# Optimization experiments

Measured on AMD Instinct MI355X. Metric: run time of the kernel, lower is better.

## Reference

```python
import jax, jax.numpy as jnp
import numpy as np

T, D, H, E, TOP_K = 4096, 512, 2048, 16, 2


def setup_inputs() -> dict:
    key = jax.random.key(0)
    ks = jax.random.split(key, 4)
    x = jax.random.normal(ks[0], (T, D), dtype=jnp.float32)
    Wg = jax.random.normal(ks[1], (D, E), dtype=jnp.float32) * 0.02
    bg = jnp.zeros((E,), dtype=jnp.float32)
    W1 = jax.random.normal(ks[2], (E, D, H), dtype=jnp.float32) * 0.02
    b1 = jnp.zeros((E, H), dtype=jnp.float32)
    W2 = jax.random.normal(ks[3], (E, H, D), dtype=jnp.float32) * 0.02
    b2 = jnp.zeros((E, D), dtype=jnp.float32)
    return {"x": x, "Wg": Wg, "bg": bg, "W1": W1, "b1": b1, "W2": W2, "b2": b2}


def reference(x, Wg, bg, W1, b1, W2, b2):
    # NaiveGate: linear -> top-k -> softmax over the k selected logits
    logits = x @ Wg + bg                               # [T, E]
    gate_vals, gate_idx = jax.lax.top_k(logits, TOP_K)  # [T, k]
    gate_score = jax.nn.softmax(gate_vals, axis=-1)     # returned by gate; NOT applied to output (faithful to source)

    # combine weights: how many top-k slots of each token map to each expert
    counts = jax.nn.one_hot(gate_idx, E, dtype=x.dtype).sum(axis=1)  # [T, E]

    # Expert FFN (grouped GEMM expressed densely over the fixed expert axis)
    h = jax.nn.gelu(jnp.einsum('td,edh->eth', x, W1) + b1[:, None, :])  # [E, T, H]
    y = jnp.einsum('eth,ehd->etd', h, W2) + b2[:, None, :]              # [E, T, D]

    # Combine: unweighted sum over the token's top-k experts (matches .sum(dim=1) in source)
    out = jnp.einsum('etd,te->td', y, counts)                            # [T, D]
    return out, gate_idx, gate_score
```

## Files before the change

### kernel.cpp

```cpp
#include <hip/hip_runtime.h>
#include <math.h>

#define T_ 4096
#define D_ 512
#define H_ 2048
#define E_ 16
#define RCAP 10240

typedef short bf16x8 __attribute__((ext_vector_type(8)));
typedef float f32x4 __attribute__((ext_vector_type(4)));

__device__ __forceinline__ unsigned short f2bf(float f) {
  union { float f; unsigned u; } v; v.f = f;
  unsigned r = v.u + 0x7fffu + ((v.u >> 16) & 1u);
  return (unsigned short)(r >> 16);
}
__device__ __forceinline__ float bf2f(unsigned short u) {
  union { unsigned u; float f; } v; v.u = ((unsigned)u) << 16;
  return v.f;
}
__device__ __forceinline__ void gload_lds16(const unsigned short* g, unsigned short* l) {
  __builtin_amdgcn_global_load_lds((const __attribute__((address_space(1))) void*)g,
                                   (__attribute__((address_space(3))) void*)l, 16, 0, 0);
}
__device__ __forceinline__ float gelu_fast(float y) {
  float s2 = 1.5957691216f * (y + 0.044715f * y * y * y);
  return y * __builtin_amdgcn_rcpf(1.f + __expf(-s2));
}

__global__ __launch_bounds__(256) void gate_kernel(const float* __restrict__ x,
                                                   const float* __restrict__ Wg,
                                                   const float* __restrict__ bg,
                                                   float* __restrict__ out,
                                                   int* __restrict__ tok2e) {
  __shared__ float wgl[D_ * E_];
  for (int i = threadIdx.x; i < D_ * E_ / 4; i += 256)
    *(float4*)&wgl[i * 4] = ((const float4*)Wg)[i];
  __syncthreads();
  const int lane = threadIdx.x & 63;
  const int t = blockIdx.x * 4 + (threadIdx.x >> 6);
  const int e = lane & 15, q = lane >> 4;
  const float4* x4 = (const float4*)(x + (size_t)t * D_ + q * 128);
  float acc = 0.f;
#pragma unroll 4
  for (int i = 0; i < 32; ++i) {
    float4 v = x4[i];
    const float* wp = &wgl[(q * 128 + i * 4) * E_ + e];
    acc += v.x * wp[0];
    acc += v.y * wp[E_];
    acc += v.z * wp[2 * E_];
    acc += v.w * wp[3 * E_];
  }
  acc += __shfl_xor(acc, 16);
  acc += __shfl_xor(acc, 32);
  const float logit = acc + bg[e];
  float v1 = logit; int i1 = e;
#pragma unroll
  for (int s = 1; s < 16; s <<= 1) {
    float ov = __shfl_xor(v1, s); int oi = __shfl_xor(i1, s);
    if (ov > v1 || (ov == v1 && oi < i1)) { v1 = ov; i1 = oi; }
  }
  float v2 = (e == i1) ? -INFINITY : logit; int i2 = e;
#pragma unroll
  for (int s = 1; s < 16; s <<= 1) {
    float ov = __shfl_xor(v2, s); int oi = __shfl_xor(i2, s);
    if (ov > v2 || (ov == v2 && oi < i2)) { v2 = ov; i2 = oi; }
  }
  if (lane == 0) {
    const float ed = __expf(v2 - v1);
    const float inv = 1.f / (1.f + ed);
    const size_t gidx = (size_t)T_ * D_;
    out[gidx + t * 2]     = (float)i1;
    out[gidx + t * 2 + 1] = (float)i2;
    out[gidx + T_ * 2 + t * 2]     = inv;
    out[gidx + T_ * 2 + t * 2 + 1] = ed * inv;
    tok2e[t * 2] = i1; tok2e[t * 2 + 1] = i2;
  }
}

__global__ void count_kernel(const int* __restrict__ tok2e,
                             int* __restrict__ cnt2,
                             int* __restrict__ offs, int* __restrict__ tileoff) {
  __shared__ int h[E_];
  if (threadIdx.x < E_) h[threadIdx.x] = 0;
  __syncthreads();
  for (int i = threadIdx.x; i < 2 * T_; i += 256) atomicAdd(&h[tok2e[i]], 1);
  __syncthreads();
  if (threadIdx.x == 0) {
    int o = 0, to = 0;
    offs[0] = 0; tileoff[0] = 0;
    for (int e = 0; e < E_; ++e) {
      int mt = (h[e] + 127) >> 7;
      o += mt << 7; to += mt;
      offs[e + 1] = o; tileoff[e + 1] = to;
    }
  }
  for (int i = threadIdx.x; i < E_ * 16; i += 256) cnt2[i] = 0;
}

__global__ __launch_bounds__(256) void scatgath_kernel(
    const float* __restrict__ x, const int* __restrict__ tok2e,
    int* __restrict__ cnt2, const int* __restrict__ offs,
    int* __restrict__ tok2row, unsigned short* __restrict__ xg) {
  const int lane = threadIdx.x & 63;
  const int t = blockIdx.x * 4 + (threadIdx.x >> 6);
  int rA = 0, rB = 0;
  if (lane == 0) {
    const int e1 = tok2e[t * 2], e2 = tok2e[t * 2 + 1];
    rA = offs[e1] + atomicAdd(&cnt2[e1 * 16], 1);
    rB = offs[e2] + atomicAdd(&cnt2[e2 * 16], 1);
    tok2row[t * 2] = rA; tok2row[t * 2 + 1] = rB;
  }
  rA = __shfl(rA, 0); rB = __shfl(rB, 0);
  const float4* p = (const float4*)(x + (size_t)t * D_ + lane * 8);
  const float4 a = p[0], b = p[1];
  const unsigned w0 = f2bf(a.x) | (f2bf(a.y) << 16);
  const unsigned w1 = f2bf(a.z) | (f2bf(a.w) << 16);
  const unsigned w2 = f2bf(b.x) | (f2bf(b.y) << 16);
  const unsigned w3 = f2bf(b.z) | (f2bf(b.w) << 16);
  const uint4 val = make_uint4(w0, w1, w2, w3);
  *(uint4*)(xg + (size_t)rA * D_ + lane * 8) = val;
  *(uint4*)(xg + (size_t)rB * D_ + lane * 8) = val;
}

template <int K, int N>
__global__ __launch_bounds__(256) void wtrans_kernel(const float* __restrict__ src,
                                                     unsigned short* __restrict__ dst) {
  __shared__ unsigned short tile[64][72];
  const int e = blockIdx.z;
  const int n0 = blockIdx.x << 6, k0 = blockIdx.y << 6;
  const int tid = threadIdx.x;
  const int tr = tid >> 4, tc = (tid & 15) << 2;
  const float* s = src + ((size_t)e * K + k0) * N + n0;
#pragma unroll
  for (int p = 0; p < 4; ++p) {
    float4 v = *(const float4*)(s + (size_t)(tr + p * 16) * N + tc);
    tile[tc + 0][tr + p * 16] = f2bf(v.x);
    tile[tc + 1][tr + p * 16] = f2bf(v.y);
    tile[tc + 2][tr + p * 16] = f2bf(v.z);
    tile[tc + 3][tr + p * 16] = f2bf(v.w);
  }
  __syncthreads();
  const int wr = tid >> 2, wc = (tid & 3) << 4;
  unsigned short* d = dst + ((size_t)e * N + n0 + wr) * K + k0 + wc;
  *(uint4*)d       = *(const uint4*)&tile[wr][wc];
  *(uint4*)(d + 8) = *(const uint4*)&tile[wr][wc + 8];
}

template <int KDIM, int NTOT, int NTILE, bool GELU>
__global__ __launch_bounds__(512, 4) void ffn_gemm(
    const unsigned short* __restrict__ A_g, const unsigned short* __restrict__ Bt_g,
    const float* __restrict__ bias_g, unsigned short* __restrict__ out_g,
    const int* __restrict__ offs, const int* __restrict__ tileoff) {
  constexpr int JN = NTILE / 64;
  constexpr int BRPW = NTILE / 8;
  constexpr int NK = KDIM / 64;
  constexpr int NBN = NTOT / NTILE;
  constexpr int NBLK = 80 * NBN;
  __shared__ unsigned short As[2 * 128 * 64];
  __shared__ unsigned short Bs[2 * NTILE * 64];
  const int lid = blockIdx.x;
  const int swz = (lid & 7) * (NBLK >> 3) + (lid >> 3);
  const int mt = swz / NBN;
  const int n0 = (swz % NBN) * NTILE;
  if (mt >= tileoff[16]) return;
  int e = 0;
  while (tileoff[e + 1] <= mt) ++e;
  const int row0 = offs[e] + ((mt - tileoff[e]) << 7);
  const int tid = threadIdx.x;
  const int lane = tid & 63;
  const int w = tid >> 6;
  const int m_off = (w >> 2) << 6;
  const int n_off = (w & 3) * (NTILE / 4);

  f32x4 acc[4][JN];
#pragma unroll
  for (int i = 0; i < 4; ++i)
#pragma unroll
    for (int j = 0; j < JN; ++j) acc[i][j] = (f32x4){0.f, 0.f, 0.f, 0.f};

  const int r_in = lane >> 3;
  const int cbg = (lane & 7) ^ r_in;
  const unsigned short* gA = A_g + (size_t)(row0 + w * 16 + r_in) * KDIM + cbg * 8;
  const unsigned short* gB = Bt_g + ((size_t)e * NTOT + n0 + w * BRPW + r_in) * KDIM + cbg * 8;

  const int q = lane >> 4, fr = lane & 15;

  auto stage = [&](int half, int k0) {
    unsigned short* lA = &As[half * (128 * 64) + w * 16 * 64];
    unsigned short* lB = &Bs[half * (NTILE * 64) + w * BRPW * 64];
#pragma unroll
    for (int j = 0; j < 2; ++j)
      gload_lds16(gA + (size_t)j * 8 * KDIM + k0, lA + j * 8 * 64);
#pragma unroll
    for (int j = 0; j < BRPW / 8; ++j)
      gload_lds16(gB + (size_t)j * 8 * KDIM + k0, lB + j * 8 * 64);
  };

  stage(0, 0);
  __syncthreads();

#pragma unroll 2
  for (int t = 0; t < NK; ++t) {
    const int cur = t & 1;
    if (t + 1 < NK) stage(cur ^ 1, (t + 1) * 64);
    const unsigned short* cA = &As[cur * (128 * 64)];
    const unsigned short* cB = &Bs[cur * (NTILE * 64)];
#pragma unroll
    for (int kk = 0; kk < 64; kk += 32) {
      bf16x8 af[4], bfr[JN];
#pragma unroll
      for (int i = 0; i < 4; ++i) {
        const int r = m_off + i * 16 + fr;
        const int sw = ((((kk >> 3) + q) ^ (r & 7)) << 3);
        af[i] = *(const bf16x8*)&cA[r * 64 + sw];
      }
#pragma unroll
      for (int j = 0; j < JN; ++j) {
        const int r = n_off + j * 16 + fr;
        const int sw = ((((kk >> 3) + q) ^ (r & 7)) << 3);
        bfr[j] = *(const bf16x8*)&cB[r * 64 + sw];
      }
#pragma unroll
      for (int i = 0; i < 4; ++i)
#pragma unroll
        for (int j = 0; j < JN; ++j)
          acc[i][j] = __builtin_amdgcn_mfma_f32_16x16x32_bf16(af[i], bfr[j], acc[i][j], 0, 0, 0);
    }
    __syncthreads();
  }

  constexpr int W = NTILE / 4;
  constexpr int LB = W / 8;
  unsigned short* cbase = &As[w * 64 * W];
  const float* bias = bias_g + (size_t)e * NTOT;
#pragma unroll
  for (int j = 0; j < JN; ++j) {
    const float bv = bias[n0 + n_off + j * 16 + fr];
#pragma unroll
    for (int i = 0; i < 4; ++i) {
      f32x4 v = acc[i][j];
#pragma unroll
      for (int r = 0; r < 4; ++r) {
        float y = v[r] + bv;
        if (GELU) y = gelu_fast(y);
        const int lr = i * 16 + (q << 2) + r;
        const int lc = j * 16 + fr;
        const int phys = (lc >> 3) ^ (lr & (LB - 1));
        cbase[lr * W + phys * 8 + (lc & 7)] = f2bf(y);
      }
    }
  }
  __syncthreads();
#pragma unroll
  for (int it = 0; it < LB; ++it) {
    const int lr = it * (64 / LB) + (lane / LB);
    const int bl = lane % LB;
    const int phys = bl ^ (lr & (LB - 1));
    const uint4 val = *(const uint4*)&cbase[lr * W + phys * 8];
    *(uint4*)&out_g[(size_t)(row0 + m_off + lr) * NTOT + n0 + n_off + bl * 8] = val;
  }
}

__global__ void combine_kernel(const unsigned short* __restrict__ ybuf,
                               const int* __restrict__ tok2row,
                               float* __restrict__ out) {
  const int t = blockIdx.x, lane = threadIdx.x;
  const int rA = tok2row[t * 2], rB = tok2row[t * 2 + 1];
  const uint4 va = *(const uint4*)(ybuf + (size_t)rA * D_ + lane * 8);
  const uint4 vb = *(const uint4*)(ybuf + (size_t)rB * D_ + lane * 8);
  const unsigned short* pa = (const unsigned short*)&va;
  const unsigned short* pb = (const unsigned short*)&vb;
  float o[8];
#pragma unroll
  for (int i = 0; i < 8; ++i) o[i] = bf2f(pa[i]) + bf2f(pb[i]);
  float4* po = (float4*)(out + (size_t)t * D_ + lane * 8);
  po[0] = make_float4(o[0], o[1], o[2], o[3]);
  po[1] = make_float4(o[4], o[5], o[6], o[7]);
}

extern "C" void kernel_launch(void* const* d_in, const int* in_sizes, int n_in,
                              void* d_out, int out_size, void* d_ws, size_t ws_size,
                              hipStream_t stream) {
  const float* x  = (const float*)d_in[0];
  const float* Wg = (const float*)d_in[1];
  const float* bg = (const float*)d_in[2];
  const float* W1 = (const float*)d_in[3];
  const float* b1 = (const float*)d_in[4];
  const float* W2 = (const float*)d_in[5];
  const float* b2 = (const float*)d_in[6];
  float* out = (float*)d_out;
  char* ws = (char*)d_ws;

  int* cnt2    = (int*)(ws);
  int* offs    = (int*)(ws + 2048);
  int* tileoff = (int*)(ws + 3072);
  int* tok2e   = (int*)(ws + 4096);
  int* tok2row = (int*)(ws + 4096 + 32768);
  unsigned short* xg   = (unsigned short*)(ws + (1 << 20));
  unsigned short* ybuf = xg;
  unsigned short* hbuf = (unsigned short*)(ws + (size_t)(12 << 20));
  unsigned short* Wt   = (unsigned short*)(ws + (size_t)(52 << 20));

  wtrans_kernel<D_, H_><<<dim3(H_ / 64, D_ / 64, E_), 256, 0, stream>>>(W1, Wt);
  gate_kernel<<<T_ / 4, 256, 0, stream>>>(x, Wg, bg, out, tok2e);
  count_kernel<<<1, 256, 0, stream>>>(tok2e, cnt2, offs, tileoff);
  scatgath_kernel<<<T_ / 4, 256, 0, stream>>>(x, tok2e, cnt2, offs, tok2row, xg);
  ffn_gemm<512, 2048, 128, true><<<1280, 512, 0, stream>>>(xg, Wt, b1, hbuf, offs, tileoff);
  wtrans_kernel<H_, D_><<<dim3(D_ / 64, H_ / 64, E_), 256, 0, stream>>>(W2, Wt);
  ffn_gemm<2048, 512, 64, false><<<640, 512, 0, stream>>>(hbuf, Wt, b2, ybuf, offs, tileoff);
  combine_kernel<<<T_, 64, 0, stream>>>(ybuf, tok2row, out);
}
```

Before: 282.2 us.

## Fuse gate with W1 transpose, fold expert counting into scatter, precompute tile map

```diff
diff --git a/kernel.cpp b/kernel.cpp
--- a/kernel.cpp
+++ b/kernel.cpp
@@ -5,7 +5,6 @@
 #define D_ 512
 #define H_ 2048
 #define E_ 16
-#define RCAP 10240
 
 typedef short bf16x8 __attribute__((ext_vector_type(8)));
 typedef float f32x4 __attribute__((ext_vector_type(4)));
@@ -28,17 +27,53 @@
   return y * __builtin_amdgcn_rcpf(1.f + __expf(-s2));
 }
 
-__global__ __launch_bounds__(256) void gate_kernel(const float* __restrict__ x,
-                                                   const float* __restrict__ Wg,
-                                                   const float* __restrict__ bg,
-                                                   float* __restrict__ out,
-                                                   int* __restrict__ tok2e) {
+template <int K, int N>
+__device__ __forceinline__ void wtrans_tile(const float* __restrict__ src,
+                                            unsigned short* __restrict__ dst,
+                                            int e, int n0, int k0, int tid,
+                                            unsigned short (*tile)[72]) {
+  const int tr = tid >> 4, tc = (tid & 15) << 2;
+  const float* s = src + ((size_t)e * K + k0) * N + n0;
+#pragma unroll
+  for (int p = 0; p < 4; ++p) {
+    float4 v = *(const float4*)(s + (size_t)(tr + p * 16) * N + tc);
+    tile[tc + 0][tr + p * 16] = f2bf(v.x);
+    tile[tc + 1][tr + p * 16] = f2bf(v.y);
+    tile[tc + 2][tr + p * 16] = f2bf(v.z);
+    tile[tc + 3][tr + p * 16] = f2bf(v.w);
+  }
+  __syncthreads();
+  const int wr = tid >> 2, wc = (tid & 3) << 4;
+  unsigned short* d = dst + ((size_t)e * N + n0 + wr) * K + k0 + wc;
+  *(uint4*)d       = *(const uint4*)&tile[wr][wc];
+  *(uint4*)(d + 8) = *(const uint4*)&tile[wr][wc + 8];
+  __syncthreads();
+}
+
+__global__ __launch_bounds__(256) void gate_wt1(
+    const float* __restrict__ x, const float* __restrict__ Wg,
+    const float* __restrict__ bg, const float* __restrict__ W1,
+    float* __restrict__ out, int* __restrict__ tok2e,
+    int* __restrict__ cnt2, unsigned short* __restrict__ Wt) {
   __shared__ float wgl[D_ * E_];
-  for (int i = threadIdx.x; i < D_ * E_ / 4; i += 256)
+  const int bid = blockIdx.x;
+  const int tid = threadIdx.x;
+  if (bid < 1024) {
+    unsigned short (*tile)[72] = (unsigned short (*)[72])wgl;
+#pragma unroll
+    for (int p = 0; p < 4; ++p) {
+      const int tt = bid + (p << 10);
+      const int we = tt >> 8, rem = tt & 255;
+      wtrans_tile<D_, H_>(W1, Wt, we, (rem & 31) << 6, (rem >> 5) << 6, tid, tile);
+    }
+    return;
+  }
+  if (bid == 1024 && tid < E_ * 16) cnt2[tid] = 0;
+  for (int i = tid; i < D_ * E_ / 4; i += 256)
     *(float4*)&wgl[i * 4] = ((const float4*)Wg)[i];
   __syncthreads();
-  const int lane = threadIdx.x & 63;
-  const int t = blockIdx.x * 4 + (threadIdx.x >> 6);
+  const int lane = tid & 63;
+  const int t = (bid - 1024) * 4 + (tid >> 6);
   const int e = lane & 15, q = lane >> 4;
   const float4* x4 = (const float4*)(x + (size_t)t * D_ + q * 128);
   float acc = 0.f;
@@ -78,37 +113,56 @@
   }
 }
 
-__global__ void count_kernel(const int* __restrict__ tok2e,
-                             int* __restrict__ cnt2,
-                             int* __restrict__ offs, int* __restrict__ tileoff) {
-  __shared__ int h[E_];
-  if (threadIdx.x < E_) h[threadIdx.x] = 0;
-  __syncthreads();
-  for (int i = threadIdx.x; i < 2 * T_; i += 256) atomicAdd(&h[tok2e[i]], 1);
-  __syncthreads();
-  if (threadIdx.x == 0) {
-    int o = 0, to = 0;
-    offs[0] = 0; tileoff[0] = 0;
-    for (int e = 0; e < E_; ++e) {
-      int mt = (h[e] + 127) >> 7;
-      o += mt << 7; to += mt;
-      offs[e + 1] = o; tileoff[e + 1] = to;
-    }
-  }
-  for (int i = threadIdx.x; i < E_ * 16; i += 256) cnt2[i] = 0;
-}
-
 __global__ __launch_bounds__(256) void scatgath_kernel(
     const float* __restrict__ x, const int* __restrict__ tok2e,
-    int* __restrict__ cnt2, const int* __restrict__ offs,
-    int* __restrict__ tok2row, unsigned short* __restrict__ xg) {
-  const int lane = threadIdx.x & 63;
-  const int t = blockIdx.x * 4 + (threadIdx.x >> 6);
+    int* __restrict__ cnt2, int* __restrict__ tok2row,
+    unsigned short* __restrict__ xg, int* __restrict__ ntiles,
+    int* __restrict__ tile2e, int* __restrict__ tile2row0) {
+  __shared__ int wsh[4][E_];
+  __shared__ int hsh[E_];
+  const int tid = threadIdx.x, lane = tid & 63, wv = tid >> 6;
+  int c[E_];
+#pragma unroll
+  for (int e = 0; e < E_; ++e) c[e] = 0;
+  for (int i = tid; i < 2 * T_; i += 256) {
+    const int v = tok2e[i];
+#pragma unroll
+    for (int e = 0; e < E_; ++e) c[e] += (v == e) ? 1 : 0;
+  }
+#pragma unroll
+  for (int e = 0; e < E_; ++e) {
+#pragma unroll
+    for (int s = 1; s < 64; s <<= 1) c[e] += __shfl_xor(c[e], s);
+  }
+  if (lane == 0) {
+#pragma unroll
+    for (int e = 0; e < E_; ++e) wsh[wv][e] = c[e];
+  }
+  __syncthreads();
+  if (tid < E_) hsh[tid] = wsh[0][tid] + wsh[1][tid] + wsh[2][tid] + wsh[3][tid];
+  __syncthreads();
+  if (blockIdx.x == 0 && tid == 0) {
+    int o = 0, to = 0;
+    for (int ee = 0; ee < E_; ++ee) {
+      const int mt = (hsh[ee] + 127) >> 7;
+      for (int i = 0; i < mt; ++i) { tile2e[to + i] = ee; tile2row0[to + i] = o + (i << 7); }
+      o += mt << 7; to += mt;
+    }
+    ntiles[0] = to;
+  }
+  const int t = blockIdx.x * 4 + wv;
   int rA = 0, rB = 0;
   if (lane == 0) {
     const int e1 = tok2e[t * 2], e2 = tok2e[t * 2 + 1];
-    rA = offs[e1] + atomicAdd(&cnt2[e1 * 16], 1);
-    rB = offs[e2] + atomicAdd(&cnt2[e2 * 16], 1);
+    int o = 0, oA = 0, oB = 0;
+#pragma unroll
+    for (int i = 0; i < E_; ++i) {
+      if (i == e1) oA = o;
+      if (i == e2) oB = o;
+      o += ((hsh[i] + 127) >> 7) << 7;
+    }
+    rA = oA + atomicAdd(&cnt2[e1 * 16], 1);
+    rB = oB + atomicAdd(&cnt2[e2 * 16], 1);
     tok2row[t * 2] = rA; tok2row[t * 2 + 1] = rB;
   }
   rA = __shfl(rA, 0); rB = __shfl(rB, 0);
@@ -123,35 +177,23 @@
   *(uint4*)(xg + (size_t)rB * D_ + lane * 8) = val;
 }
 
-template <int K, int N>
-__global__ __launch_bounds__(256) void wtrans_kernel(const float* __restrict__ src,
-                                                     unsigned short* __restrict__ dst) {
+__global__ __launch_bounds__(256) void wt2_kernel(const float* __restrict__ W2,
+                                                  unsigned short* __restrict__ Wt) {
   __shared__ unsigned short tile[64][72];
-  const int e = blockIdx.z;
-  const int n0 = blockIdx.x << 6, k0 = blockIdx.y << 6;
-  const int tid = threadIdx.x;
-  const int tr = tid >> 4, tc = (tid & 15) << 2;
-  const float* s = src + ((size_t)e * K + k0) * N + n0;
 #pragma unroll
   for (int p = 0; p < 4; ++p) {
-    float4 v = *(const float4*)(s + (size_t)(tr + p * 16) * N + tc);
-    tile[tc + 0][tr + p * 16] = f2bf(v.x);
-    tile[tc + 1][tr + p * 16] = f2bf(v.y);
-    tile[tc + 2][tr + p * 16] = f2bf(v.z);
-    tile[tc + 3][tr + p * 16] = f2bf(v.w);
-  }
-  __syncthreads();
-  const int wr = tid >> 2, wc = (tid & 3) << 4;
-  unsigned short* d = dst + ((size_t)e * N + n0 + wr) * K + k0 + wc;
-  *(uint4*)d       = *(const uint4*)&tile[wr][wc];
-  *(uint4*)(d + 8) = *(const uint4*)&tile[wr][wc + 8];
+    const int tt = blockIdx.x + (p << 10);
+    const int we = tt >> 8, rem = tt & 255;
+    wtrans_tile<H_, D_>(W2, Wt, we, (rem & 7) << 6, (rem >> 3) << 6, threadIdx.x, tile);
+  }
 }
 
 template <int KDIM, int NTOT, int NTILE, bool GELU>
 __global__ __launch_bounds__(512, 4) void ffn_gemm(
     const unsigned short* __restrict__ A_g, const unsigned short* __restrict__ Bt_g,
     const float* __restrict__ bias_g, unsigned short* __restrict__ out_g,
-    const int* __restrict__ offs, const int* __restrict__ tileoff) {
+    const int* __restrict__ ntiles, const int* __restrict__ tile2e,
+    const int* __restrict__ tile2row0) {
   constexpr int JN = NTILE / 64;
   constexpr int BRPW = NTILE / 8;
   constexpr int NK = KDIM / 64;
@@ -163,10 +205,9 @@
   const int swz = (lid & 7) * (NBLK >> 3) + (lid >> 3);
   const int mt = swz / NBN;
   const int n0 = (swz % NBN) * NTILE;
-  if (mt >= tileoff[16]) return;
-  int e = 0;
-  while (tileoff[e + 1] <= mt) ++e;
-  const int row0 = offs[e] + ((mt - tileoff[e]) << 7);
+  if (mt >= ntiles[0]) return;
+  const int e = tile2e[mt];
+  const int row0 = tile2row0[mt];
   const int tid = threadIdx.x;
   const int lane = tid & 63;
   const int w = tid >> 6;
@@ -183,7 +224,6 @@
   const int cbg = (lane & 7) ^ r_in;
   const unsigned short* gA = A_g + (size_t)(row0 + w * 16 + r_in) * KDIM + cbg * 8;
   const unsigned short* gB = Bt_g + ((size_t)e * NTOT + n0 + w * BRPW + r_in) * KDIM + cbg * 8;
-
   const int q = lane >> 4, fr = lane & 15;
 
   auto stage = [&](int half, int k0) {
@@ -262,10 +302,11 @@
   }
 }
 
-__global__ void combine_kernel(const unsigned short* __restrict__ ybuf,
-                               const int* __restrict__ tok2row,
-                               float* __restrict__ out) {
-  const int t = blockIdx.x, lane = threadIdx.x;
+__global__ __launch_bounds__(512) void combine_kernel(
+    const unsigned short* __restrict__ ybuf, const int* __restrict__ tok2row,
+    float* __restrict__ out) {
+  const int lane = threadIdx.x & 63;
+  const int t = blockIdx.x * 8 + (threadIdx.x >> 6);
   const int rA = tok2row[t * 2], rB = tok2row[t * 2 + 1];
   const uint4 va = *(const uint4*)(ybuf + (size_t)rA * D_ + lane * 8);
   const uint4 vb = *(const uint4*)(ybuf + (size_t)rB * D_ + lane * 8);
@@ -292,22 +333,24 @@
   float* out = (float*)d_out;
   char* ws = (char*)d_ws;
 
-  int* cnt2    = (int*)(ws);
-  int* offs    = (int*)(ws + 2048);
-  int* tileoff = (int*)(ws + 3072);
-  int* tok2e   = (int*)(ws + 4096);
-  int* tok2row = (int*)(ws + 4096 + 32768);
+  int* cnt2      = (int*)(ws);
+  int* ntiles    = (int*)(ws + 2112);
+  int* tile2e    = (int*)(ws + 2176);
+  int* tile2row0 = (int*)(ws + 2560);
+  int* tok2e     = (int*)(ws + 4096);
+  int* tok2row   = (int*)(ws + 4096 + 32768);
   unsigned short* xg   = (unsigned short*)(ws + (1 << 20));
   unsigned short* ybuf = xg;
   unsigned short* hbuf = (unsigned short*)(ws + (size_t)(12 << 20));
   unsigned short* Wt   = (unsigned short*)(ws + (size_t)(52 << 20));
 
-  wtrans_kernel<D_, H_><<<dim3(H_ / 64, D_ / 64, E_), 256, 0, stream>>>(W1, Wt);
-  gate_kernel<<<T_ / 4, 256, 0, stream>>>(x, Wg, bg, out, tok2e);
-  count_kernel<<<1, 256, 0, stream>>>(tok2e, cnt2, offs, tileoff);
-  scatgath_kernel<<<T_ / 4, 256, 0, stream>>>(x, tok2e, cnt2, offs, tok2row, xg);
-  ffn_gemm<512, 2048, 128, true><<<1280, 512, 0, stream>>>(xg, Wt, b1, hbuf, offs, tileoff);
-  wtrans_kernel<H_, D_><<<dim3(D_ / 64, H_ / 64, E_), 256, 0, stream>>>(W2, Wt);
-  ffn_gemm<2048, 512, 64, false><<<640, 512, 0, stream>>>(hbuf, Wt, b2, ybuf, offs, tileoff);
-  combine_kernel<<<T_, 64, 0, stream>>>(ybuf, tok2row, out);
-}
+  gate_wt1<<<2048, 256, 0, stream>>>(x, Wg, bg, W1, out, tok2e, cnt2, Wt);
+  scatgath_kernel<<<T_ / 4, 256, 0, stream>>>(x, tok2e, cnt2, tok2row, xg,
+                                              ntiles, tile2e, tile2row0);
+  ffn_gemm<512, 2048, 128, true><<<1280, 512, 0, stream>>>(
+      xg, Wt, b1, hbuf, ntiles, tile2e, tile2row0);
+  wt2_kernel<<<1024, 256, 0, stream>>>(W2, Wt);
+  ffn_gemm<2048, 512, 64, false><<<640, 512, 0, stream>>>(
+      hbuf, Wt, b2, ybuf, ntiles, tile2e, tile2row0);
+  combine_kernel<<<512, 512, 0, stream>>>(ybuf, tok2row, out);
+}
```

Result: no change. 282.0 us (-0.1%).
